# Performance work log

Hardware: AMD Instinct MI355X
Metric: run time of the kernel (lower is better)

The kernel has to match this reference:

```python
import jax, jax.numpy as jnp
import numpy as np

B, C, IN_H, IN_W = 32, 16, 64, 64
OUT_H, OUT_W, K, STRIDE = 60, 60, 5, 1


def setup_inputs() -> dict:
    key = jax.random.key(0)
    k1, k2 = jax.random.split(key)
    # spike-like inputs in [0,1)
    in_spikes = jax.random.uniform(k1, (B, C, IN_H, IN_W), dtype=jnp.float32)
    # unshared locally-connected weights: (outH, outW, C_in, K, K, C_out)
    weights = jax.random.normal(k2, (OUT_H, OUT_W, C, K, K, C), dtype=jnp.float32) * (1.0 / (K * K))
    return {"in_spikes": in_spikes, "weights": weights}


def _extract_patches(x, out_h, out_w, k, stride):
    # x: (B, C, H, W) -> patches: (B, C, K, K, out_h, out_w)
    # static K*K loop over kernel offsets (not a data-dim loop)
    rows = []
    for di in range(k):
        cols = []
        for dj in range(k):
            cols.append(x[:, :, di:di + out_h * stride:stride, dj:dj + out_w * stride:stride])
        rows.append(jnp.stack(cols, axis=2))  # (B, C, K, out_h, out_w)
    return jnp.stack(rows, axis=2)  # (B, C, K, K, out_h, out_w)


def reference(in_spikes, weights):
    out_h, out_w, _, k, _, _ = weights.shape
    patches = _extract_patches(in_spikes, out_h, out_w, k, STRIDE)
    # output[b, k_out, i, j] = sum_{c,u,v} patches[b,c,u,v,i,j] * weights[i,j,c,u,v,k_out]
    out = jnp.einsum('bcuvij,ijcuvk->bkij', patches, weights)
    return out
```

## Files before the change

### kernel.cpp

```cpp
#include <hip/hip_runtime.h>
#include <hip/hip_bf16.h>


#define OUT_HW 60
#define IN_HW  64
#define CIN    16
#define COUT   16
#define NPOS   3600
#define BK     512
#define XC_ELE (32u * 64u * 64u * 16u)

typedef __attribute__((ext_vector_type(8))) short bf16x8;
typedef __attribute__((ext_vector_type(4))) float f32x4;

static __device__ __forceinline__ unsigned pk2(float a, float b) {
    union { __hip_bfloat162 h; unsigned u; } cv;
    cv.h = __float22bfloat162_rn(make_float2(a, b));
    return cv.u;
}

static __device__ __forceinline__ void g2lds16(const float* g, float* l) {
    __builtin_amdgcn_global_load_lds(
        (const __attribute__((address_space(1))) unsigned int*)g,
        (__attribute__((address_space(3))) unsigned int*)l, 16, 0, 0);
}

__global__ __launch_bounds__(256)
void make_xc(const float* __restrict__ x, ushort* __restrict__ xc) {
    const int bh = blockIdx.x;
    const int b = bh >> 6, h = bh & 63;
    const int t = threadIdx.x;
    const int cq = t & 3, wc = t >> 2;
    const float* src = x + ((size_t)(b * CIN) * IN_HW + h) * IN_HW + wc;
    float f[4];
#pragma unroll
    for (int e = 0; e < 4; ++e)
        f[e] = src[(size_t)(cq * 4 + e) * (IN_HW * IN_HW)];
    union { ushort4 v; unsigned u[2]; } o;
    o.u[0] = pk2(f[0], f[1]);
    o.u[1] = pk2(f[2], f[3]);
    *(ushort4*)&xc[((size_t)bh * IN_HW + wc) * CIN + cq * 4] = o.v;
}

template<int PACKED>
__global__ __launch_bounds__(256, 4)
void lc_pos(const ushort* __restrict__ xc, const float* __restrict__ w,
            float* __restrict__ dst) {
    __shared__ float sWraw[6400] __attribute__((aligned(16)));
    __shared__ float sRed[4][32 * 17];

    const int bid = blockIdx.x;
    const int pos = (bid & 7) * 450 + (bid >> 3);
    const int i = pos / OUT_HW, j = pos - i * OUT_HW;
    const int t = threadIdx.x;
    const int lane = t & 63, wv = t >> 6;
    const int l15 = lane & 15, q = lane >> 4;
    const int qh = q >> 1, c0 = (q & 1) << 3;

    const float* wsrc = w + (size_t)pos * 6400 + lane * 4;
    for (int o = wv; o < 25; o += 4)
        g2lds16(wsrc + o * 256, &sWraw[o * 256]);

    const int base_hw = i * IN_HW + j;
    bf16x8 xa0[4], xa1[4];
#pragma unroll
    for (int it = 0; it < 4; ++it) {
        const int cc = wv + it * 4;
        if (cc < 13) {
            const int uvB = cc * 2 + qh;
            const int uvA = (uvB < 25) ? uvB : 24;
            const int uA = (uvA * 13) >> 6;
            const int vA = uvA - 5 * uA;
            const size_t xoff = (size_t)l15 * (IN_HW * IN_HW * CIN)
                              + (size_t)(base_hw + uA * IN_HW + vA) * CIN + c0;
            xa0[it] = *(const bf16x8*)(xc + xoff);
            xa1[it] = *(const bf16x8*)(xc + xoff + 16u * IN_HW * IN_HW * CIN);
        }
    }

    __syncthreads();

    f32x4 acc0 = {0.f, 0.f, 0.f, 0.f}, acc1 = {0.f, 0.f, 0.f, 0.f};
#pragma unroll
    for (int it = 0; it < 4; ++it) {
        const int cc = wv + it * 4;
        if (cc < 13) {
            const int uvB = cc * 2 + qh;
            const int okB = (uvB < 25);
            float bfv[8];
#pragma unroll
            for (int jj = 0; jj < 8; ++jj)
                bfv[jj] = okB ? sWraw[(c0 + jj) * 400 + uvB * 16 + l15] : 0.f;
            union { bf16x8 v; unsigned u[4]; } pb;
#pragma unroll
            for (int jj = 0; jj < 4; ++jj) pb.u[jj] = pk2(bfv[2 * jj], bfv[2 * jj + 1]);
            acc0 = __builtin_amdgcn_mfma_f32_16x16x32_bf16(xa0[it], pb.v, acc0, 0, 0, 0);
            acc1 = __builtin_amdgcn_mfma_f32_16x16x32_bf16(xa1[it], pb.v, acc1, 0, 0, 0);
        }
    }

#pragma unroll
    for (int r = 0; r < 4; ++r) {
        sRed[wv][(q * 4 + r) * 17 + l15]      = acc0[r];
        sRed[wv][(q * 4 + r + 16) * 17 + l15] = acc1[r];
    }
    __syncthreads();
#pragma unroll
    for (int h = 0; h < 2; ++h) {
        const int o = t + h * 256;
        const int idx = (o >> 4) * 17 + (o & 15);
        const float sv = sRed[0][idx] + sRed[1][idx] + sRed[2][idx] + sRed[3][idx];
        if (PACKED) dst[(size_t)pos * BK + o] = sv;
        else        dst[(size_t)o * NPOS + pos] = sv;
    }
}

__global__ __launch_bounds__(256)
void transpose_out(const float* __restrict__ src, float* __restrict__ out) {
    __shared__ float tile[64][65];
    const int o0 = blockIdx.x * 64;
    const int k0 = blockIdx.y * 64;
    const int t  = threadIdx.x;
    const int tx = t & 63, ty = t >> 6;
    for (int r = ty; r < 64; r += 4) {
        const int oij = o0 + r;
        if (oij < NPOS) tile[r][tx] = src[(size_t)oij * BK + k0 + tx];
    }
    __syncthreads();
    for (int r = ty; r < 64; r += 4) {
        const int oij = o0 + tx;
        if (oij < NPOS) out[(size_t)(k0 + r) * NPOS + oij] = tile[tx][r];
    }
}

__global__ __launch_bounds__(256)
void lc_naive(const float* __restrict__ x, const float* __restrict__ w,
              float* __restrict__ out) {
    const int gid = blockIdx.x * 256 + threadIdx.x;
    if (gid >= 32 * COUT * NPOS) return;
    const int j = gid % OUT_HW;
    int rest = gid / OUT_HW;
    const int i = rest % OUT_HW; rest /= OUT_HW;
    const int k = rest % COUT;
    const int b = rest / COUT;
    const float* wp = w + (size_t)(i * OUT_HW + j) * 6400 + k;
    float s = 0.f;
    for (int c = 0; c < CIN; ++c)
        for (int u = 0; u < 5; ++u)
            for (int v = 0; v < 5; ++v)
                s += x[((size_t)(b * CIN + c) * IN_HW + i + u) * IN_HW + j + v]
                   * wp[((c * 5 + u) * 5 + v) * COUT];
    out[gid] = s;
}

extern "C" void kernel_launch(void* const* d_in, const int* in_sizes, int n_in,
                              void* d_out, int out_size, void* d_ws, size_t ws_size,
                              hipStream_t stream) {
    const float* x = (const float*)d_in[0];
    const float* w = (const float*)d_in[1];
    float* out = (float*)d_out;

    const size_t xcBytes  = (size_t)XC_ELE * 2;
    const size_t outBytes = (size_t)NPOS * BK * 4;
    ushort* xc = (ushort*)d_ws;

    if (ws_size >= xcBytes + outBytes) {
        float* wsOut = (float*)((char*)d_ws + xcBytes);
        make_xc<<<32 * IN_HW, 256, 0, stream>>>(x, xc);
        lc_pos<1><<<NPOS, 256, 0, stream>>>(xc, w, wsOut);
        transpose_out<<<dim3((NPOS + 63) / 64, BK / 64), 256, 0, stream>>>(wsOut, out);
    } else if (ws_size >= xcBytes) {
        make_xc<<<32 * IN_HW, 256, 0, stream>>>(x, xc);
        lc_pos<0><<<NPOS, 256, 0, stream>>>(xc, w, out);
    } else {
        lc_naive<<<(32 * COUT * NPOS + 255) / 256, 256, 0, stream>>>(x, w, out);
    }
}
```

Baseline: 155.7 us.

## Map one output position per wave and write transposed output directly

Each wave now computes a whole output position on its own, running all 13 K-chunks with weights read straight from global memory rather than staged through LDS, so 900 blocks each cover 4 adjacent positions. Blocks store their 4 positions as a float4 per output row, which removes the intermediate packed buffer and the separate transpose kernel. The aim is to drop one kernel launch, an extra global round trip and the cross-wave LDS reduction. In exchange, weight loads become uncoalesced strided scalar reads, there is less parallelism per position, and the XCD remapping assumes a particular scheduling pattern.

```diff
diff --git a/kernel.cpp b/kernel.cpp
--- a/kernel.cpp
+++ b/kernel.cpp
@@ -7,7 +7,6 @@
 #define CIN    16
 #define COUT   16
 #define NPOS   3600
-#define BK     512
 #define XC_ELE (32u * 64u * 64u * 16u)
 
 typedef __attribute__((ext_vector_type(8))) short bf16x8;
@@ -17,12 +16,6 @@
     union { __hip_bfloat162 h; unsigned u; } cv;
     cv.h = __float22bfloat162_rn(make_float2(a, b));
     return cv.u;
-}
-
-static __device__ __forceinline__ void g2lds16(const float* g, float* l) {
-    __builtin_amdgcn_global_load_lds(
-        (const __attribute__((address_space(1))) unsigned int*)g,
-        (__attribute__((address_space(3))) unsigned int*)l, 16, 0, 0);
 }
 
 __global__ __launch_bounds__(256)
@@ -42,94 +35,66 @@
     *(ushort4*)&xc[((size_t)bh * IN_HW + wc) * CIN + cq * 4] = o.v;
 }
 
-template<int PACKED>
 __global__ __launch_bounds__(256, 4)
-void lc_pos(const ushort* __restrict__ xc, const float* __restrict__ w,
-            float* __restrict__ dst) {
-    __shared__ float sWraw[6400] __attribute__((aligned(16)));
-    __shared__ float sRed[4][32 * 17];
+void lc_wave(const ushort* __restrict__ xc, const float* __restrict__ w,
+             float* __restrict__ out) {
+    __shared__ float sOut[4][512];
 
     const int bid = blockIdx.x;
-    const int pos = (bid & 7) * 450 + (bid >> 3);
-    const int i = pos / OUT_HW, j = pos - i * OUT_HW;
+    const int xcd = bid & 7, ii = bid >> 3;
+    const int wg = (xcd < 4 ? xcd * 113 : 452 + (xcd - 4) * 112) + ii;
+
     const int t = threadIdx.x;
     const int lane = t & 63, wv = t >> 6;
+    const int pos = wg * 4 + wv;
+    const int i = pos / OUT_HW, j = pos - i * OUT_HW;
     const int l15 = lane & 15, q = lane >> 4;
-    const int qh = q >> 1, c0 = (q & 1) << 3;
+    const int qh = q >> 1;
+    const int ch = (q & 1) << 3;
 
-    const float* wsrc = w + (size_t)pos * 6400 + lane * 4;
-    for (int o = wv; o < 25; o += 4)
-        g2lds16(wsrc + o * 256, &sWraw[o * 256]);
+    const float* wp = w + (size_t)pos * 6400 + (ch * 25 + qh) * 16 + l15;
 
     const int base_hw = i * IN_HW + j;
-    bf16x8 xa0[4], xa1[4];
-#pragma unroll
-    for (int it = 0; it < 4; ++it) {
-        const int cc = wv + it * 4;
-        if (cc < 13) {
-            const int uvB = cc * 2 + qh;
-            const int uvA = (uvB < 25) ? uvB : 24;
-            const int uA = (uvA * 13) >> 6;
-            const int vA = uvA - 5 * uA;
-            const size_t xoff = (size_t)l15 * (IN_HW * IN_HW * CIN)
-                              + (size_t)(base_hw + uA * IN_HW + vA) * CIN + c0;
-            xa0[it] = *(const bf16x8*)(xc + xoff);
-            xa1[it] = *(const bf16x8*)(xc + xoff + 16u * IN_HW * IN_HW * CIN);
-        }
-    }
-
-    __syncthreads();
+    const ushort* xb = xc + (size_t)l15 * (IN_HW * IN_HW * CIN) + ch;
 
     f32x4 acc0 = {0.f, 0.f, 0.f, 0.f}, acc1 = {0.f, 0.f, 0.f, 0.f};
 #pragma unroll
-    for (int it = 0; it < 4; ++it) {
-        const int cc = wv + it * 4;
-        if (cc < 13) {
-            const int uvB = cc * 2 + qh;
-            const int okB = (uvB < 25);
-            float bfv[8];
+    for (int cc = 0; cc < 13; ++cc) {
+        const int uv = cc * 2 + qh;
+        const int ok = (uv < 25);
+        const int uvc = ok ? uv : 24;
+        const int u = (uvc * 13) >> 6;
+        const int v = uvc - 5 * u;
+
+        const ushort* xp = xb + (size_t)(base_hw + u * IN_HW + v) * CIN;
+        bf16x8 a0 = *(const bf16x8*)xp;
+        bf16x8 a1 = *(const bf16x8*)(xp + 16u * IN_HW * IN_HW * CIN);
+
+        float bw[8];
 #pragma unroll
-            for (int jj = 0; jj < 8; ++jj)
-                bfv[jj] = okB ? sWraw[(c0 + jj) * 400 + uvB * 16 + l15] : 0.f;
-            union { bf16x8 v; unsigned u[4]; } pb;
+        for (int jj = 0; jj < 8; ++jj)
+            bw[jj] = ok ? wp[jj * 400 + cc * 32] : 0.f;
+        union { bf16x8 v; unsigned u[4]; } pb;
 #pragma unroll
-            for (int jj = 0; jj < 4; ++jj) pb.u[jj] = pk2(bfv[2 * jj], bfv[2 * jj + 1]);
-            acc0 = __builtin_amdgcn_mfma_f32_16x16x32_bf16(xa0[it], pb.v, acc0, 0, 0, 0);
-            acc1 = __builtin_amdgcn_mfma_f32_16x16x32_bf16(xa1[it], pb.v, acc1, 0, 0, 0);
-        }
+        for (int jj = 0; jj < 4; ++jj)
+            pb.u[jj] = pk2(bw[2 * jj], bw[2 * jj + 1]);
+
+        acc0 = __builtin_amdgcn_mfma_f32_16x16x32_bf16(a0, pb.v, acc0, 0, 0, 0);
+        acc1 = __builtin_amdgcn_mfma_f32_16x16x32_bf16(a1, pb.v, acc1, 0, 0, 0);
     }
 
 #pragma unroll
     for (int r = 0; r < 4; ++r) {
-        sRed[wv][(q * 4 + r) * 17 + l15]      = acc0[r];
-        sRed[wv][(q * 4 + r + 16) * 17 + l15] = acc1[r];
+        sOut[wv][(q * 4 + r) * 16 + l15]      = acc0[r];
+        sOut[wv][(q * 4 + r + 16) * 16 + l15] = acc1[r];
     }
     __syncthreads();
+    const int p0 = wg * 4;
 #pragma unroll
     for (int h = 0; h < 2; ++h) {
         const int o = t + h * 256;
-        const int idx = (o >> 4) * 17 + (o & 15);
-        const float sv = sRed[0][idx] + sRed[1][idx] + sRed[2][idx] + sRed[3][idx];
-        if (PACKED) dst[(size_t)pos * BK + o] = sv;
-        else        dst[(size_t)o * NPOS + pos] = sv;
-    }
-}
-
-__global__ __launch_bounds__(256)
-void transpose_out(const float* __restrict__ src, float* __restrict__ out) {
-    __shared__ float tile[64][65];
-    const int o0 = blockIdx.x * 64;
-    const int k0 = blockIdx.y * 64;
-    const int t  = threadIdx.x;
-    const int tx = t & 63, ty = t >> 6;
-    for (int r = ty; r < 64; r += 4) {
-        const int oij = o0 + r;
-        if (oij < NPOS) tile[r][tx] = src[(size_t)oij * BK + k0 + tx];
-    }
-    __syncthreads();
-    for (int r = ty; r < 64; r += 4) {
-        const int oij = o0 + tx;
-        if (oij < NPOS) out[(size_t)(k0 + r) * NPOS + oij] = tile[tx][r];
+        f32x4 vo = { sOut[0][o], sOut[1][o], sOut[2][o], sOut[3][o] };
+        *(f32x4*)(out + (size_t)o * NPOS + p0) = vo;
     }
 }
 
@@ -160,18 +125,12 @@
     const float* w = (const float*)d_in[1];
     float* out = (float*)d_out;
 
-    const size_t xcBytes  = (size_t)XC_ELE * 2;
-    const size_t outBytes = (size_t)NPOS * BK * 4;
-    ushort* xc = (ushort*)d_ws;
+    const size_t xcBytes = (size_t)XC_ELE * 2;
 
-    if (ws_size >= xcBytes + outBytes) {
-        float* wsOut = (float*)((char*)d_ws + xcBytes);
+    if (ws_size >= xcBytes) {
+        ushort* xc = (ushort*)d_ws;
         make_xc<<<32 * IN_HW, 256, 0, stream>>>(x, xc);
-        lc_pos<1><<<NPOS, 256, 0, stream>>>(xc, w, wsOut);
-        transpose_out<<<dim3((NPOS + 63) / 64, BK / 64), 256, 0, stream>>>(wsOut, out);
-    } else if (ws_size >= xcBytes) {
-        make_xc<<<32 * IN_HW, 256, 0, stream>>>(x, xc);
-        lc_pos<0><<<NPOS, 256, 0, stream>>>(xc, w, out);
+        lc_wave<<<900, 256, 0, stream>>>(xc, w, out);
     } else {
         lc_naive<<<(32 * COUT * NPOS + 255) / 256, 256, 0, stream>>>(x, w, out);
     }
```

Result: no change. 155.4 us (-0.2%).
